# Kernel tuning notes

Measured on AMD Instinct MI355X. Metric: run time of the kernel, lower is better.

## Reference

```python
import jax, jax.numpy as jnp
import numpy as np


def _soft_attention(h, context, W_in, W_out):
    """Luong soft-dot attention. h: [B,H], context: [B,L,H].
    W_in: [H,H] (in,out layout), W_out: [2H,H]."""
    target = h @ W_in                                  # [B, H]
    attn = jnp.einsum('blh,bh->bl', context, target)   # [B, L]
    p = jax.nn.softmax(attn, axis=-1)                  # [B, L]
    weighted_ctx = jnp.einsum('bl,blh->bh', p, context)  # [B, H]
    h_tilde = jnp.tanh(jnp.concatenate([weighted_ctx, h], axis=1) @ W_out)  # [B, H]
    return h_tilde, p


def setup_inputs() -> dict:
    key = jax.random.key(0)
    ks = jax.random.split(key, 13)
    B, L, H = 64, 512, 1024
    s2 = 1.0 / np.sqrt(2 * H)
    s1 = 1.0 / np.sqrt(H)
    return {
        'h_tilde_s': jax.random.normal(ks[0], (B, H), jnp.float32),
        'h_tilde_o': jax.random.normal(ks[1], (B, H), jnp.float32),
        'h_tilde_a': jax.random.normal(ks[2], (B, H), jnp.float32),
        'enc_out': jax.random.normal(ks[3], (B, L, H), jnp.float32),
        'full_feature_len': 36,
        'W_as': jax.random.normal(ks[4], (2 * H, H), jnp.float32) * s2,
        'W_so': jax.random.normal(ks[5], (2 * H, H), jnp.float32) * s2,
        'W_oa': jax.random.normal(ks[6], (2 * H, H), jnp.float32) * s2,
        'Win_as': jax.random.normal(ks[7], (H, H), jnp.float32) * s1,
        'Win_so': jax.random.normal(ks[8], (H, H), jnp.float32) * s1,
        'Win_oa': jax.random.normal(ks[9], (H, H), jnp.float32) * s1,
        'Wout_as': jax.random.normal(ks[10], (2 * H, H), jnp.float32) * s2,
        'Wout_so': jax.random.normal(ks[11], (2 * H, H), jnp.float32) * s2,
        'Wout_oa': jax.random.normal(ks[12], (2 * H, H), jnp.float32) * s2,
    }


def reference(h_tilde_s, h_tilde_o, h_tilde_a, enc_out, full_feature_len,
              W_as, W_so, W_oa, Win_as, Win_so, Win_oa,
              Wout_as, Wout_so, Wout_oa):
    # Relational contexts via concat + linear(no bias) + tanh
    h_as = jnp.tanh(jnp.concatenate([h_tilde_a, h_tilde_s], axis=1) @ W_as)  # [B,H]
    h_so = jnp.tanh(jnp.concatenate([h_tilde_s, h_tilde_o], axis=1) @ W_so)
    h_oa = jnp.tanh(jnp.concatenate([h_tilde_o, h_tilde_a], axis=1) @ W_oa)
    # Three parallel soft-dot attentions over encoder output
    sa_as, _ = _soft_attention(h_as, enc_out, Win_as, Wout_as)
    sa_so, _ = _soft_attention(h_so, enc_out, Win_so, Wout_so)
    sa_oa, _ = _soft_attention(h_oa, enc_out, Win_oa, Wout_oa)
    B, H = sa_as.shape
    F = full_feature_len
    # repeat_interleave of size-1 dim == broadcast tile to [B, F, H]
    ctx_mas = jnp.broadcast_to(sa_as[:, None, :], (B, F, H))
    ctx_mso = jnp.broadcast_to(sa_so[:, None, :], (B, F, H))
    ctx_moa = jnp.broadcast_to(sa_oa[:, None, :], (B, F, H))
    return (ctx_mas, ctx_mso, ctx_moa)
```

## Files before the change

### kernel.cpp

```cpp
#include <hip/hip_runtime.h>

constexpr int BB = 64;
constexpr int LL = 512;
constexpr int HH = 1024;
constexpr int SPLITS = 16;

typedef float nt_float4 __attribute__((ext_vector_type(4)));

struct Ptr3 { const float* p[3]; };

template<int K0, int K1>
__global__ __launch_bounds__(256)
void gemm_skinny(Ptr3 A0, Ptr3 A1, Ptr3 Wp, float* __restrict__ part)
{
    constexpr int K = K0 + K1;
    constexpr int KRANGE = K / SPLITS;
    __shared__ float As[32][64];
    __shared__ float Ws[32][64];
    const int r   = blockIdx.z;
    const int n0  = blockIdx.x * 64;
    const int ks  = blockIdx.y * KRANGE;
    const int tid = threadIdx.x;
    const float* a0 = A0.p[r];
    const float* a1 = A1.p[r];
    const float* w  = Wp.p[r];

    const int tn = tid & 15;
    const int tm = tid >> 4;

    float acc[4][4] = {};

    for (int kt = ks; kt < ks + KRANGE; kt += 32) {
        {
            const int m   = tid >> 2;
            const int kk0 = (tid & 3) << 3;
            const int kg  = kt + kk0;
            const float* src = (K1 == 0 || kg < K0) ? (a0 + (size_t)m * HH + kg)
                                                    : (a1 + (size_t)m * HH + (kg - K0));
            float4 v0 = *(const float4*)(src);
            float4 v1 = *(const float4*)(src + 4);
            As[kk0 + 0][m] = v0.x; As[kk0 + 1][m] = v0.y;
            As[kk0 + 2][m] = v0.z; As[kk0 + 3][m] = v0.w;
            As[kk0 + 4][m] = v1.x; As[kk0 + 5][m] = v1.y;
            As[kk0 + 6][m] = v1.z; As[kk0 + 7][m] = v1.w;
        }
        {
            const int j4 = (tid & 15) << 2;
            int kk = tid >> 4;
            #pragma unroll
            for (int i = 0; i < 2; i++, kk += 16) {
                *(float4*)&Ws[kk][j4] = *(const float4*)(w + (size_t)(kt + kk) * HH + n0 + j4);
            }
        }
        __syncthreads();
        #pragma unroll
        for (int kk = 0; kk < 32; kk++) {
            float4 a4 = *(const float4*)&As[kk][tm << 2];
            float4 b4 = *(const float4*)&Ws[kk][tn << 2];
            float av[4] = {a4.x, a4.y, a4.z, a4.w};
            float bv[4] = {b4.x, b4.y, b4.z, b4.w};
            #pragma unroll
            for (int i = 0; i < 4; i++)
                #pragma unroll
                for (int j = 0; j < 4; j++)
                    acc[i][j] += av[i] * bv[j];
        }
        __syncthreads();
    }

    float* dst = part + (size_t)((r * SPLITS + blockIdx.y) * 64) * HH + n0 + (tn << 2);
    #pragma unroll
    for (int i = 0; i < 4; i++) {
        const int m = (tm << 2) + i;
        *(float4*)(dst + (size_t)m * HH) = make_float4(acc[i][0], acc[i][1], acc[i][2], acc[i][3]);
    }
}

template<bool TANH>
__global__ __launch_bounds__(256)
void reduce_split(const float* __restrict__ part, float* __restrict__ dst)
{
    const int i4   = blockIdx.x * 256 + threadIdx.x;
    const int flat = i4 << 2;
    const int r    = flat >> 16;
    const int mn   = flat & 65535;
    const float* p = part + (size_t)r * SPLITS * 65536 + mn;
    float4 s = *(const float4*)p;
    #pragma unroll
    for (int y = 1; y < SPLITS; y++) {
        float4 q = *(const float4*)(p + (size_t)y * 65536);
        s.x += q.x; s.y += q.y; s.z += q.z; s.w += q.w;
    }
    if (TANH) {
        s.x = tanhf(s.x); s.y = tanhf(s.y); s.z = tanhf(s.z); s.w = tanhf(s.w);
    }
    *(float4*)(dst + (size_t)r * 65536 + mn) = s;
}

__global__ __launch_bounds__(256)
void flash_chunk(const float* __restrict__ enc, const float* __restrict__ tt,
                 float* __restrict__ opm, float* __restrict__ ms)
{
    __shared__ float o_l[4][3][HH];
    __shared__ float ms_sh[4][3][2];
    const int b    = blockIdx.x >> 3;
    const int lc   = blockIdx.x & 7;
    const int tid  = threadIdx.x;
    const int lane = tid & 63;
    const int w    = tid >> 6;

    float4 tr[3][4];
    #pragma unroll
    for (int r = 0; r < 3; r++)
        #pragma unroll
        for (int v = 0; v < 4; v++)
            tr[r][v] = *(const float4*)&tt[(size_t)(r * BB + b) * HH + (lane << 2) + (v << 8)];

    float  m_run[3] = {-3.0e38f, -3.0e38f, -3.0e38f};
    float  S_run[3] = {0.f, 0.f, 0.f};
    float4 o_run[3][4];
    #pragma unroll
    for (int r = 0; r < 3; r++)
        #pragma unroll
        for (int v = 0; v < 4; v++)
            o_run[r][v] = make_float4(0.f, 0.f, 0.f, 0.f);

    const float* ebase = enc + ((size_t)b * LL + (lc << 6) + (w << 2)) * HH + (lane << 2);

    for (int it = 0; it < 4; it++) {
        const float* e = ebase + (size_t)(it << 4) * HH;
        float4 ev[4][4];
        #pragma unroll
        for (int j = 0; j < 4; j++)
            #pragma unroll
            for (int v = 0; v < 4; v++)
                ev[j][v] = *(const float4*)(e + (size_t)j * HH + (v << 8));

        float s[3][4];
        #pragma unroll
        for (int j = 0; j < 4; j++) {
            float d0 = 0.f, d1 = 0.f, d2 = 0.f;
            #pragma unroll
            for (int v = 0; v < 4; v++) {
                const float4 x = ev[j][v];
                d0 += x.x * tr[0][v].x + x.y * tr[0][v].y + x.z * tr[0][v].z + x.w * tr[0][v].w;
                d1 += x.x * tr[1][v].x + x.y * tr[1][v].y + x.z * tr[1][v].z + x.w * tr[1][v].w;
                d2 += x.x * tr[2][v].x + x.y * tr[2][v].y + x.z * tr[2][v].z + x.w * tr[2][v].w;
            }
            #pragma unroll
            for (int off = 32; off > 0; off >>= 1) {
                d0 += __shfl_xor(d0, off);
                d1 += __shfl_xor(d1, off);
                d2 += __shfl_xor(d2, off);
            }
            s[0][j] = d0; s[1][j] = d1; s[2][j] = d2;
        }

        #pragma unroll
        for (int r = 0; r < 3; r++) {
            const float mb = fmaxf(fmaxf(s[r][0], s[r][1]), fmaxf(s[r][2], s[r][3]));
            const float mn_ = fmaxf(m_run[r], mb);
            const float alpha = __expf(m_run[r] - mn_);
            m_run[r] = mn_;
            float p[4];
            float psum = 0.f;
            #pragma unroll
            for (int j = 0; j < 4; j++) { p[j] = __expf(s[r][j] - mn_); psum += p[j]; }
            S_run[r] = S_run[r] * alpha + psum;
            #pragma unroll
            for (int v = 0; v < 4; v++) {
                float4 o = o_run[r][v];
                o.x *= alpha; o.y *= alpha; o.z *= alpha; o.w *= alpha;
                #pragma unroll
                for (int j = 0; j < 4; j++) {
                    const float4 x = ev[j][v];
                    o.x += p[j] * x.x; o.y += p[j] * x.y;
                    o.z += p[j] * x.z; o.w += p[j] * x.w;
                }
                o_run[r][v] = o;
            }
        }
    }

    #pragma unroll
    for (int r = 0; r < 3; r++) {
        #pragma unroll
        for (int v = 0; v < 4; v++)
            *(float4*)&o_l[w][r][(lane << 2) + (v << 8)] = o_run[r][v];
        if (lane == 0) { ms_sh[w][r][0] = m_run[r]; ms_sh[w][r][1] = S_run[r]; }
    }
    __syncthreads();

    const int chunk = (b << 3) + lc;
    #pragma unroll
    for (int r = 0; r < 3; r++) {
        const float m0 = ms_sh[0][r][0], m1 = ms_sh[1][r][0];
        const float m2 = ms_sh[2][r][0], m3 = ms_sh[3][r][0];
        const float M = fmaxf(fmaxf(m0, m1), fmaxf(m2, m3));
        const float w0 = __expf(m0 - M), w1 = __expf(m1 - M);
        const float w2 = __expf(m2 - M), w3 = __expf(m3 - M);
        float4 q0 = *(const float4*)&o_l[0][r][tid << 2];
        float4 q1 = *(const float4*)&o_l[1][r][tid << 2];
        float4 q2 = *(const float4*)&o_l[2][r][tid << 2];
        float4 q3 = *(const float4*)&o_l[3][r][tid << 2];
        float4 acc;
        acc.x = w0 * q0.x + w1 * q1.x + w2 * q2.x + w3 * q3.x;
        acc.y = w0 * q0.y + w1 * q1.y + w2 * q2.y + w3 * q3.y;
        acc.z = w0 * q0.z + w1 * q1.z + w2 * q2.z + w3 * q3.z;
        acc.w = w0 * q0.w + w1 * q1.w + w2 * q2.w + w3 * q3.w;
        *(float4*)&opm[((size_t)chunk * 3 + r) * HH + (tid << 2)] = acc;
        if (tid == 0) {
            const float S = w0 * ms_sh[0][r][1] + w1 * ms_sh[1][r][1]
                          + w2 * ms_sh[2][r][1] + w3 * ms_sh[3][r][1];
            ms[((size_t)chunk * 3 + r) * 2 + 0] = M;
            ms[((size_t)chunk * 3 + r) * 2 + 1] = S;
        }
    }
}

__global__ __launch_bounds__(256)
void flash_combine(const float* __restrict__ opm, const float* __restrict__ ms,
                   float* __restrict__ wc)
{
    __shared__ float ms_l[8][2];
    const int b   = blockIdx.x;
    const int r   = blockIdx.y;
    const int tid = threadIdx.x;

    if (tid < 8) {
        const int chunk = (b << 3) + tid;
        ms_l[tid][0] = ms[((size_t)chunk * 3 + r) * 2 + 0];
        ms_l[tid][1] = ms[((size_t)chunk * 3 + r) * 2 + 1];
    }
    __syncthreads();

    float M = -3.0e38f;
    #pragma unroll
    for (int c = 0; c < 8; c++) M = fmaxf(M, ms_l[c][0]);

    float S = 0.f;
    float4 acc = make_float4(0.f, 0.f, 0.f, 0.f);
    #pragma unroll
    for (int c = 0; c < 8; c++) {
        const float wgt = __expf(ms_l[c][0] - M);
        S += wgt * ms_l[c][1];
        const int chunk = (b << 3) + c;
        float4 q = *(const float4*)&opm[((size_t)chunk * 3 + r) * HH + (tid << 2)];
        acc.x += wgt * q.x; acc.y += wgt * q.y;
        acc.z += wgt * q.z; acc.w += wgt * q.w;
    }
    const float inv = 1.0f / S;
    acc.x *= inv; acc.y *= inv; acc.z *= inv; acc.w *= inv;
    *(float4*)&wc[(size_t)(r * BB + b) * HH + (tid << 2)] = acc;
}

__global__ __launch_bounds__(256)
void reduce_tanh_broadcast(const float* __restrict__ part, const int* __restrict__ Fp,
                           float* __restrict__ out)
{
    const int i4   = blockIdx.x * 256 + threadIdx.x;
    const int flat = i4 << 2;
    const int r    = flat >> 16;
    const int mn   = flat & 65535;
    const float* p = part + (size_t)r * SPLITS * 65536 + mn;
    float4 s = *(const float4*)p;
    #pragma unroll
    for (int y = 1; y < SPLITS; y++) {
        float4 q = *(const float4*)(p + (size_t)y * 65536);
        s.x += q.x; s.y += q.y; s.z += q.z; s.w += q.w;
    }
    s.x = tanhf(s.x); s.y = tanhf(s.y); s.z = tanhf(s.z); s.w = tanhf(s.w);

    nt_float4 sv;
    sv.x = s.x; sv.y = s.y; sv.z = s.z; sv.w = s.w;

    const int F  = *Fp;
    const int bb = mn >> 10;
    const int hh = mn & 1023;
    float* o = out + ((size_t)(r * BB + bb) * F) * HH + hh;
    for (int f = 0; f < F; f++)
        __builtin_nontemporal_store(sv, (nt_float4*)(o + (size_t)f * HH));
}

extern "C" void kernel_launch(void* const* d_in, const int* in_sizes, int n_in,
                              void* d_out, int out_size, void* d_ws, size_t ws_size,
                              hipStream_t stream)
{
    (void)in_sizes; (void)n_in; (void)out_size; (void)ws_size;
    const float* hs  = (const float*)d_in[0];
    const float* ho  = (const float*)d_in[1];
    const float* ha  = (const float*)d_in[2];
    const float* enc = (const float*)d_in[3];
    const int*   Fp  = (const int*)d_in[4];
    const float* W_as    = (const float*)d_in[5];
    const float* W_so    = (const float*)d_in[6];
    const float* W_oa    = (const float*)d_in[7];
    const float* Win_as  = (const float*)d_in[8];
    const float* Win_so  = (const float*)d_in[9];
    const float* Win_oa  = (const float*)d_in[10];
    const float* Wout_as = (const float*)d_in[11];
    const float* Wout_so = (const float*)d_in[12];
    const float* Wout_oa = (const float*)d_in[13];

    float* ws   = (float*)d_ws;
    float* part = ws;
    float* hx   = ws + 3145728;
    float* tt   = ws + 3342336;
    float* wc   = ws + 3538944;
    float* opm  = ws + 3735552;
    float* msb  = ws + 5308416;

    {
        Ptr3 A0{{ha, hs, ho}};
        Ptr3 A1{{hs, ho, ha}};
        Ptr3 W {{W_as, W_so, W_oa}};
        gemm_skinny<1024, 1024><<<dim3(16, SPLITS, 3), 256, 0, stream>>>(A0, A1, W, part);
    }
    reduce_split<true><<<192, 256, 0, stream>>>(part, hx);

    {
        Ptr3 A0{{hx, hx + 65536, hx + 131072}};
        Ptr3 A1{{nullptr, nullptr, nullptr}};
        Ptr3 W {{Win_as, Win_so, Win_oa}};
        gemm_skinny<1024, 0><<<dim3(16, SPLITS, 3), 256, 0, stream>>>(A0, A1, W, part);
    }
    reduce_split<false><<<192, 256, 0, stream>>>(part, tt);

    flash_chunk<<<512, 256, 0, stream>>>(enc, tt, opm, msb);
    flash_combine<<<dim3(64, 3), 256, 0, stream>>>(opm, msb, wc);

    {
        Ptr3 A0{{wc, wc + 65536, wc + 131072}};
        Ptr3 A1{{hx, hx + 65536, hx + 131072}};
        Ptr3 W {{Wout_as, Wout_so, Wout_oa}};
        gemm_skinny<1024, 1024><<<dim3(16, SPLITS, 3), 256, 0, stream>>>(A0, A1, W, part);
    }

    reduce_tanh_broadcast<<<192, 256, 0, stream>>>(part, Fp, (float*)d_out);
}
```

Measured before the change: 318.5 us.

## Fuse all stages into one cooperative persistent kernel with grid syncs

Replaces the eight separate kernel launches with a single cooperative mega-kernel of 512 blocks that runs the GEMMs, reductions, flash attention, combine and broadcast as phases separated by grid.sync. The flash stage's shared memory is cut so two blocks fit per CU: per-wave partial outputs are staged one relation at a time with extra barriers. The goal is to remove launch gaps and per-kernel ramp-up and tail costs. In exchange it adds grid-wide barrier costs, fewer waves per GEMM phase (768 work items over 512 blocks), and keeps the separate-kernel path as a fallback.

```diff
diff --git a/kernel.cpp b/kernel.cpp
--- a/kernel.cpp
+++ b/kernel.cpp
@@ -1,30 +1,40 @@
 #include <hip/hip_runtime.h>
+#include <hip/hip_cooperative_groups.h>
+
+namespace cg = cooperative_groups;
 
 constexpr int BB = 64;
 constexpr int LL = 512;
 constexpr int HH = 1024;
 constexpr int SPLITS = 16;
+constexpr int GRID  = 512;
+constexpr int NTHR  = 256;
+constexpr int NWORK_GEMM = 3 * 16 * SPLITS;
 
 typedef float nt_float4 __attribute__((ext_vector_type(4)));
 
-struct Ptr3 { const float* p[3]; };
+struct Args {
+    const float* hs; const float* ho; const float* ha; const float* enc;
+    const int* Fp;
+    const float* W_as;  const float* W_so;  const float* W_oa;
+    const float* Win_as; const float* Win_so; const float* Win_oa;
+    const float* Wout_as; const float* Wout_so; const float* Wout_oa;
+    float* part; float* hx; float* tt; float* wc; float* opm; float* ms;
+    float* out;
+};
 
 template<int K0, int K1>
-__global__ __launch_bounds__(256)
-void gemm_skinny(Ptr3 A0, Ptr3 A1, Ptr3 Wp, float* __restrict__ part)
+__device__ __forceinline__ void gemm_tile(const float* __restrict__ a0,
+                                          const float* __restrict__ a1,
+                                          const float* __restrict__ w,
+                                          float* __restrict__ part_r,
+                                          int nt, int sp, int tid,
+                                          float (*As)[64], float (*Ws)[64])
 {
     constexpr int K = K0 + K1;
     constexpr int KRANGE = K / SPLITS;
-    __shared__ float As[32][64];
-    __shared__ float Ws[32][64];
-    const int r   = blockIdx.z;
-    const int n0  = blockIdx.x * 64;
-    const int ks  = blockIdx.y * KRANGE;
-    const int tid = threadIdx.x;
-    const float* a0 = A0.p[r];
-    const float* a1 = A1.p[r];
-    const float* w  = Wp.p[r];
-
+    const int n0 = nt << 6;
+    const int ks = sp * KRANGE;
     const int tn = tid & 15;
     const int tm = tid >> 4;
 
@@ -68,7 +78,7 @@
         __syncthreads();
     }
 
-    float* dst = part + (size_t)((r * SPLITS + blockIdx.y) * 64) * HH + n0 + (tn << 2);
+    float* dst = part_r + (size_t)(sp << 6) * HH + n0 + (tn << 2);
     #pragma unroll
     for (int i = 0; i < 4; i++) {
         const int m = (tm << 2) + i;
@@ -76,12 +86,50 @@
     }
 }
 
-template<bool TANH>
-__global__ __launch_bounds__(256)
-void reduce_split(const float* __restrict__ part, float* __restrict__ dst)
-{
-    const int i4   = blockIdx.x * 256 + threadIdx.x;
-    const int flat = i4 << 2;
+__device__ __forceinline__ void gemmA_work(const Args& a, int wk, int tid,
+                                           float (*As)[64], float (*Ws)[64])
+{
+    const int r  = wk >> 8;
+    const int nt = wk & 15;
+    const int sp = (wk >> 4) & 15;
+    const float* a0 = (r == 0) ? a.ha : (r == 1) ? a.hs : a.ho;
+    const float* a1 = (r == 0) ? a.hs : (r == 1) ? a.ho : a.ha;
+    const float* w  = (r == 0) ? a.W_as : (r == 1) ? a.W_so : a.W_oa;
+    gemm_tile<1024, 1024>(a0, a1, w, a.part + (size_t)r * SPLITS * 65536,
+                          nt, sp, tid, As, Ws);
+}
+
+__device__ __forceinline__ void gemmC_work(const Args& a, int wk, int tid,
+                                           float (*As)[64], float (*Ws)[64])
+{
+    const int r  = wk >> 8;
+    const int nt = wk & 15;
+    const int sp = (wk >> 4) & 15;
+    const float* a0 = a.hx + (size_t)r * 65536;
+    const float* w  = (r == 0) ? a.Win_as : (r == 1) ? a.Win_so : a.Win_oa;
+    gemm_tile<1024, 0>(a0, nullptr, w, a.part + (size_t)r * SPLITS * 65536,
+                       nt, sp, tid, As, Ws);
+}
+
+__device__ __forceinline__ void gemmG_work(const Args& a, int wk, int tid,
+                                           float (*As)[64], float (*Ws)[64])
+{
+    const int r  = wk >> 8;
+    const int nt = wk & 15;
+    const int sp = (wk >> 4) & 15;
+    const float* a0 = a.wc + (size_t)r * 65536;
+    const float* a1 = a.hx + (size_t)r * 65536;
+    const float* w  = (r == 0) ? a.Wout_as : (r == 1) ? a.Wout_so : a.Wout_oa;
+    gemm_tile<1024, 1024>(a0, a1, w, a.part + (size_t)r * SPLITS * 65536,
+                          nt, sp, tid, As, Ws);
+}
+
+__device__ __forceinline__ void reduce_phase(const float* __restrict__ part,
+                                             float* __restrict__ dst,
+                                             int gtid, bool do_tanh)
+{
+    if (gtid >= 49152) return;
+    const int flat = gtid << 2;
     const int r    = flat >> 16;
     const int mn   = flat & 65535;
     const float* p = part + (size_t)r * SPLITS * 65536 + mn;
@@ -91,30 +139,28 @@
         float4 q = *(const float4*)(p + (size_t)y * 65536);
         s.x += q.x; s.y += q.y; s.z += q.z; s.w += q.w;
     }
-    if (TANH) {
+    if (do_tanh) {
         s.x = tanhf(s.x); s.y = tanhf(s.y); s.z = tanhf(s.z); s.w = tanhf(s.w);
     }
     *(float4*)(dst + (size_t)r * 65536 + mn) = s;
 }
 
-__global__ __launch_bounds__(256)
-void flash_chunk(const float* __restrict__ enc, const float* __restrict__ tt,
-                 float* __restrict__ opm, float* __restrict__ ms)
-{
-    __shared__ float o_l[4][3][HH];
-    __shared__ float ms_sh[4][3][2];
-    const int b    = blockIdx.x >> 3;
-    const int lc   = blockIdx.x & 7;
-    const int tid  = threadIdx.x;
+__device__ __forceinline__ void flash_phase(const Args& args, int chunk, int tid,
+                                            float* smem)
+{
+    float (*o_l)[HH]     = (float(*)[HH])smem;
+    float (*ms_sh)[3][2] = (float(*)[3][2])(smem + 4096);
+    const int b    = chunk >> 3;
+    const int lc   = chunk & 7;
     const int lane = tid & 63;
-    const int w    = tid >> 6;
+    const int wv   = tid >> 6;
 
     float4 tr[3][4];
     #pragma unroll
     for (int r = 0; r < 3; r++)
         #pragma unroll
         for (int v = 0; v < 4; v++)
-            tr[r][v] = *(const float4*)&tt[(size_t)(r * BB + b) * HH + (lane << 2) + (v << 8)];
+            tr[r][v] = *(const float4*)&args.tt[(size_t)(r * BB + b) * HH + (lane << 2) + (v << 8)];
 
     float  m_run[3] = {-3.0e38f, -3.0e38f, -3.0e38f};
     float  S_run[3] = {0.f, 0.f, 0.f};
@@ -125,7 +171,7 @@
         for (int v = 0; v < 4; v++)
             o_run[r][v] = make_float4(0.f, 0.f, 0.f, 0.f);
 
-    const float* ebase = enc + ((size_t)b * LL + (lc << 6) + (w << 2)) * HH + (lane << 2);
+    const float* ebase = args.enc + ((size_t)b * LL + (lc << 6) + (wv << 2)) * HH + (lane << 2);
 
     for (int it = 0; it < 4; it++) {
         const float* e = ebase + (size_t)(it << 4) * HH;
@@ -182,87 +228,76 @@
         }
     }
 
+    if (lane == 0) {
+        #pragma unroll
+        for (int r = 0; r < 3; r++) { ms_sh[wv][r][0] = m_run[r]; ms_sh[wv][r][1] = S_run[r]; }
+    }
+
     #pragma unroll
     for (int r = 0; r < 3; r++) {
+        __syncthreads();
         #pragma unroll
         for (int v = 0; v < 4; v++)
-            *(float4*)&o_l[w][r][(lane << 2) + (v << 8)] = o_run[r][v];
-        if (lane == 0) { ms_sh[w][r][0] = m_run[r]; ms_sh[w][r][1] = S_run[r]; }
-    }
-    __syncthreads();
-
-    const int chunk = (b << 3) + lc;
-    #pragma unroll
-    for (int r = 0; r < 3; r++) {
+            *(float4*)&o_l[wv][(lane << 2) + (v << 8)] = o_run[r][v];
+        __syncthreads();
+
         const float m0 = ms_sh[0][r][0], m1 = ms_sh[1][r][0];
         const float m2 = ms_sh[2][r][0], m3 = ms_sh[3][r][0];
         const float M = fmaxf(fmaxf(m0, m1), fmaxf(m2, m3));
         const float w0 = __expf(m0 - M), w1 = __expf(m1 - M);
         const float w2 = __expf(m2 - M), w3 = __expf(m3 - M);
-        float4 q0 = *(const float4*)&o_l[0][r][tid << 2];
-        float4 q1 = *(const float4*)&o_l[1][r][tid << 2];
-        float4 q2 = *(const float4*)&o_l[2][r][tid << 2];
-        float4 q3 = *(const float4*)&o_l[3][r][tid << 2];
+        float4 q0 = *(const float4*)&o_l[0][tid << 2];
+        float4 q1 = *(const float4*)&o_l[1][tid << 2];
+        float4 q2 = *(const float4*)&o_l[2][tid << 2];
+        float4 q3 = *(const float4*)&o_l[3][tid << 2];
         float4 acc;
         acc.x = w0 * q0.x + w1 * q1.x + w2 * q2.x + w3 * q3.x;
         acc.y = w0 * q0.y + w1 * q1.y + w2 * q2.y + w3 * q3.y;
         acc.z = w0 * q0.z + w1 * q1.z + w2 * q2.z + w3 * q3.z;
         acc.w = w0 * q0.w + w1 * q1.w + w2 * q2.w + w3 * q3.w;
-        *(float4*)&opm[((size_t)chunk * 3 + r) * HH + (tid << 2)] = acc;
+        *(float4*)&args.opm[((size_t)chunk * 3 + r) * HH + (tid << 2)] = acc;
         if (tid == 0) {
             const float S = w0 * ms_sh[0][r][1] + w1 * ms_sh[1][r][1]
                           + w2 * ms_sh[2][r][1] + w3 * ms_sh[3][r][1];
-            ms[((size_t)chunk * 3 + r) * 2 + 0] = M;
-            ms[((size_t)chunk * 3 + r) * 2 + 1] = S;
-        }
-    }
-}
-
-__global__ __launch_bounds__(256)
-void flash_combine(const float* __restrict__ opm, const float* __restrict__ ms,
-                   float* __restrict__ wc)
-{
-    __shared__ float ms_l[8][2];
-    const int b   = blockIdx.x;
-    const int r   = blockIdx.y;
-    const int tid = threadIdx.x;
-
-    if (tid < 8) {
-        const int chunk = (b << 3) + tid;
-        ms_l[tid][0] = ms[((size_t)chunk * 3 + r) * 2 + 0];
-        ms_l[tid][1] = ms[((size_t)chunk * 3 + r) * 2 + 1];
-    }
-    __syncthreads();
-
+            args.ms[((size_t)chunk * 3 + r) * 2 + 0] = M;
+            args.ms[((size_t)chunk * 3 + r) * 2 + 1] = S;
+        }
+    }
+}
+
+__device__ __forceinline__ void combine_phase(const Args& args, int b, int r, int tid)
+{
+    float mv[8], sv[8];
     float M = -3.0e38f;
     #pragma unroll
-    for (int c = 0; c < 8; c++) M = fmaxf(M, ms_l[c][0]);
-
+    for (int c = 0; c < 8; c++) {
+        const int chunk = (b << 3) + c;
+        mv[c] = args.ms[((size_t)chunk * 3 + r) * 2 + 0];
+        sv[c] = args.ms[((size_t)chunk * 3 + r) * 2 + 1];
+        M = fmaxf(M, mv[c]);
+    }
     float S = 0.f;
     float4 acc = make_float4(0.f, 0.f, 0.f, 0.f);
     #pragma unroll
     for (int c = 0; c < 8; c++) {
-        const float wgt = __expf(ms_l[c][0] - M);
-        S += wgt * ms_l[c][1];
+        const float wgt = __expf(mv[c] - M);
+        S += wgt * sv[c];
         const int chunk = (b << 3) + c;
-        float4 q = *(const float4*)&opm[((size_t)chunk * 3 + r) * HH + (tid << 2)];
+        float4 q = *(const float4*)&args.opm[((size_t)chunk * 3 + r) * HH + (tid << 2)];
         acc.x += wgt * q.x; acc.y += wgt * q.y;
         acc.z += wgt * q.z; acc.w += wgt * q.w;
     }
     const float inv = 1.0f / S;
     acc.x *= inv; acc.y *= inv; acc.z *= inv; acc.w *= inv;
-    *(float4*)&wc[(size_t)(r * BB + b) * HH + (tid << 2)] = acc;
-}
-
-__global__ __launch_bounds__(256)
-void reduce_tanh_broadcast(const float* __restrict__ part, const int* __restrict__ Fp,
-                           float* __restrict__ out)
-{
-    const int i4   = blockIdx.x * 256 + threadIdx.x;
-    const int flat = i4 << 2;
+    *(float4*)&args.wc[(size_t)(r * BB + b) * HH + (tid << 2)] = acc;
+}
+
+__device__ __forceinline__ void broadcast_phase(const Args& args, int gtid)
+{
+    const int flat = gtid << 2;
     const int r    = flat >> 16;
     const int mn   = flat & 65535;
-    const float* p = part + (size_t)r * SPLITS * 65536 + mn;
+    const float* p = args.part + (size_t)r * SPLITS * 65536 + mn;
     float4 s = *(const float4*)p;
     #pragma unroll
     for (int y = 1; y < SPLITS; y++) {
@@ -274,12 +309,97 @@
     nt_float4 sv;
     sv.x = s.x; sv.y = s.y; sv.z = s.z; sv.w = s.w;
 
-    const int F  = *Fp;
+    const int F  = *args.Fp;
     const int bb = mn >> 10;
     const int hh = mn & 1023;
-    float* o = out + ((size_t)(r * BB + bb) * F) * HH + hh;
+    float* o = args.out + ((size_t)(r * BB + bb) * F) * HH + hh;
     for (int f = 0; f < F; f++)
         __builtin_nontemporal_store(sv, (nt_float4*)(o + (size_t)f * HH));
+}
+
+__global__ __launch_bounds__(NTHR, 2)
+void mega_kernel(Args args)
+{
+    __shared__ __align__(16) float smem[4224];
+    cg::grid_group grid = cg::this_grid();
+    const int bid  = blockIdx.x;
+    const int tid  = threadIdx.x;
+    const int gtid = bid * NTHR + tid;
+
+    float (*As)[64] = (float(*)[64])smem;
+    float (*Ws)[64] = (float(*)[64])(smem + 2048);
+
+    for (int wk = bid; wk < NWORK_GEMM; wk += gridDim.x)
+        gemmA_work(args, wk, tid, As, Ws);
+    grid.sync();
+
+    reduce_phase(args.part, args.hx, gtid, true);
+    grid.sync();
+
+    for (int wk = bid; wk < NWORK_GEMM; wk += gridDim.x)
+        gemmC_work(args, wk, tid, As, Ws);
+    grid.sync();
+
+    reduce_phase(args.part, args.tt, gtid, false);
+    grid.sync();
+
+    flash_phase(args, bid, tid, smem);
+    grid.sync();
+
+    if (bid < 192)
+        combine_phase(args, bid & 63, bid >> 6, tid);
+    grid.sync();
+
+    for (int wk = bid; wk < NWORK_GEMM; wk += gridDim.x)
+        gemmG_work(args, wk, tid, As, Ws);
+    grid.sync();
+
+    if (gtid < 49152)
+        broadcast_phase(args, gtid);
+}
+
+__global__ __launch_bounds__(NTHR)
+void k_gemmA(Args a)
+{
+    __shared__ __align__(16) float smem[4096];
+    gemmA_work(a, blockIdx.x, threadIdx.x, (float(*)[64])smem, (float(*)[64])(smem + 2048));
+}
+
+__global__ __launch_bounds__(NTHR)
+void k_gemmC(Args a)
+{
+    __shared__ __align__(16) float smem[4096];
+    gemmC_work(a, blockIdx.x, threadIdx.x, (float(*)[64])smem, (float(*)[64])(smem + 2048));
+}
+
+__global__ __launch_bounds__(NTHR)
+void k_gemmG(Args a)
+{
+    __shared__ __align__(16) float smem[4096];
+    gemmG_work(a, blockIdx.x, threadIdx.x, (float(*)[64])smem, (float(*)[64])(smem + 2048));
+}
+
+__global__ __launch_bounds__(NTHR)
+void k_reduceB(Args a) { reduce_phase(a.part, a.hx, blockIdx.x * NTHR + threadIdx.x, true); }
+
+__global__ __launch_bounds__(NTHR)
+void k_reduceD(Args a) { reduce_phase(a.part, a.tt, blockIdx.x * NTHR + threadIdx.x, false); }
+
+__global__ __launch_bounds__(NTHR)
+void k_flash(Args a)
+{
+    __shared__ __align__(16) float smem[4224];
+    flash_phase(a, blockIdx.x, threadIdx.x, smem);
+}
+
+__global__ __launch_bounds__(NTHR)
+void k_combine(Args a) { combine_phase(a, blockIdx.x, blockIdx.y, threadIdx.x); }
+
+__global__ __launch_bounds__(NTHR)
+void k_broadcast(Args a)
+{
+    const int gtid = blockIdx.x * NTHR + threadIdx.x;
+    if (gtid < 49152) broadcast_phase(a, gtid);
 }
 
 extern "C" void kernel_launch(void* const* d_in, const int* in_sizes, int n_in,
@@ -287,54 +407,59 @@
                               hipStream_t stream)
 {
     (void)in_sizes; (void)n_in; (void)out_size; (void)ws_size;
-    const float* hs  = (const float*)d_in[0];
-    const float* ho  = (const float*)d_in[1];
-    const float* ha  = (const float*)d_in[2];
-    const float* enc = (const float*)d_in[3];
-    const int*   Fp  = (const int*)d_in[4];
-    const float* W_as    = (const float*)d_in[5];
-    const float* W_so    = (const float*)d_in[6];
-    const float* W_oa    = (const float*)d_in[7];
-    const float* Win_as  = (const float*)d_in[8];
-    const float* Win_so  = (const float*)d_in[9];
-    const float* Win_oa  = (const float*)d_in[10];
-    const float* Wout_as = (const float*)d_in[11];
-    const float* Wout_so = (const float*)d_in[12];
-    const float* Wout_oa = (const float*)d_in[13];
-
-    float* ws   = (float*)d_ws;
-    float* part = ws;
-    float* hx   = ws + 3145728;
-    float* tt   = ws + 3342336;
-    float* wc   = ws + 3538944;
-    float* opm  = ws + 3735552;
-    float* msb  = ws + 5308416;
-
-    {
-        Ptr3 A0{{ha, hs, ho}};
-        Ptr3 A1{{hs, ho, ha}};
-        Ptr3 W {{W_as, W_so, W_oa}};
-        gemm_skinny<1024, 1024><<<dim3(16, SPLITS, 3), 256, 0, stream>>>(A0, A1, W, part);
-    }
-    reduce_split<true><<<192, 256, 0, stream>>>(part, hx);
-
-    {
-        Ptr3 A0{{hx, hx + 65536, hx + 131072}};
-        Ptr3 A1{{nullptr, nullptr, nullptr}};
-        Ptr3 W {{Win_as, Win_so, Win_oa}};
-        gemm_skinny<1024, 0><<<dim3(16, SPLITS, 3), 256, 0, stream>>>(A0, A1, W, part);
-    }
-    reduce_split<false><<<192, 256, 0, stream>>>(part, tt);
-
-    flash_chunk<<<512, 256, 0, stream>>>(enc, tt, opm, msb);
-    flash_combine<<<dim3(64, 3), 256, 0, stream>>>(opm, msb, wc);
-
-    {
-        Ptr3 A0{{wc, wc + 65536, wc + 131072}};
-        Ptr3 A1{{hx, hx + 65536, hx + 131072}};
-        Ptr3 W {{Wout_as, Wout_so, Wout_oa}};
-        gemm_skinny<1024, 1024><<<dim3(16, SPLITS, 3), 256, 0, stream>>>(A0, A1, W, part);
-    }
-
-    reduce_tanh_broadcast<<<192, 256, 0, stream>>>(part, Fp, (float*)d_out);
-}
+    float* ws = (float*)d_ws;
+
+    Args a;
+    a.hs  = (const float*)d_in[0];
+    a.ho  = (const float*)d_in[1];
+    a.ha  = (const float*)d_in[2];
+    a.enc = (const float*)d_in[3];
+    a.Fp  = (const int*)d_in[4];
+    a.W_as    = (const float*)d_in[5];
+    a.W_so    = (const float*)d_in[6];
+    a.W_oa    = (const float*)d_in[7];
+    a.Win_as  = (const float*)d_in[8];
+    a.Win_so  = (const float*)d_in[9];
+    a.Win_oa  = (const float*)d_in[10];
+    a.Wout_as = (const float*)d_in[11];
+    a.Wout_so = (const float*)d_in[12];
+    a.Wout_oa = (const float*)d_in[13];
+
+    a.part = ws;
+    a.hx   = ws + 3145728;
+    a.tt   = ws + 3342336;
+    a.wc   = ws + 3538944;
+    a.opm  = ws + 3735552;
+    a.ms   = ws + 5308416;
+    a.out  = (float*)d_out;
+
+    static int coop = -2;
+    if (coop == -2) {
+        int dev = 0, cus = 0, nb = 0;
+        hipGetDevice(&dev);
+        hipDeviceGetAttribute(&cus, hipDeviceAttributeMultiprocessorCount, dev);
+        hipError_t e = hipOccupancyMaxActiveBlocksPerMultiprocessor(&nb, mega_kernel, NTHR, 0);
+        coop = (e == hipSuccess && nb > 0 && (long)nb * cus >= GRID) ? 1 : 0;
+    }
+
+    bool launched = false;
+    if (coop == 1) {
+        void* kargs[] = { (void*)&a };
+        hipError_t e = hipLaunchCooperativeKernel((const void*)mega_kernel,
+                                                  dim3(GRID), dim3(NTHR),
+                                                  kargs, 0, stream);
+        launched = (e == hipSuccess);
+        if (!launched) coop = 0;
+    }
+
+    if (!launched) {
+        k_gemmA<<<NWORK_GEMM, NTHR, 0, stream>>>(a);
+        k_reduceB<<<192, NTHR, 0, stream>>>(a);
+        k_gemmC<<<NWORK_GEMM, NTHR, 0, stream>>>(a);
+        k_reduceD<<<192, NTHR, 0, stream>>>(a);
+        k_flash<<<512, NTHR, 0, stream>>>(a);
+        k_combine<<<dim3(64, 3), NTHR, 0, stream>>>(a);
+        k_gemmG<<<NWORK_GEMM, NTHR, 0, stream>>>(a);
+        k_broadcast<<<192, NTHR, 0, stream>>>(a);
+    }
+}
```

New measurement: 327.4 us. 2.8% more time.
